# Kernel optimization log

Hardware: AMD Instinct MI355X
Metric: run time of the kernel (lower is better)

## Reference

```python
import jax, jax.numpy as jnp
import numpy as np
from jax import lax

SIZE = 1024
INPUT_DIM = 1024
T = 8192
FORGET_BIAS = 1.0  # BasicLSTMCell default


def setup_inputs() -> dict:
    key = jax.random.key(0)
    k1, k2 = jax.random.split(key)
    x = jax.random.normal(k1, (T, INPUT_DIM), dtype=jnp.float32)
    # BasicLSTMCell kernel: [input_dim + size, 4*size], gate order [i, j, f, o]
    W = jax.random.normal(k2, (INPUT_DIM + SIZE, 4 * SIZE), dtype=jnp.float32) * 0.02
    b = jnp.zeros((4 * SIZE,), dtype=jnp.float32)
    return {"x": x, "W": W, "b": b}


def reference(x, W, b):
    size = b.shape[0] // 4
    c0 = jnp.zeros((size,), dtype=x.dtype)
    h0 = jnp.zeros((size,), dtype=x.dtype)

    def step(carry, xt):
        c, h = carry
        # concat([x_t, h_{t-1}]) @ W + b, split into 4 gates [i, j, f, o]
        z = jnp.concatenate([xt, h]) @ W + b
        i, j, f, o = jnp.split(z, 4)
        new_c = c * jax.nn.sigmoid(f + FORGET_BIAS) + jax.nn.sigmoid(i) * jnp.tanh(j)
        new_h = jnp.tanh(new_c) * jax.nn.sigmoid(o)
        return (new_c, new_h), new_h

    _, hs = lax.scan(step, (c0, h0), x)
    # tf.reshape(rnn, [-1, size]) -> [T, size]
    return hs
```

## Files before the change

kernel.cpp:

```cpp
#include <hip/hip_runtime.h>
#include <hip/hip_fp16.h>
#include <math.h>

#define T_STEPS 8192
#define IN_DIM  1024
#define HD      1024
#define ZD      4096
#define G2      64
#define B2      512

typedef short  short8 __attribute__((ext_vector_type(8)));
typedef float  f32x4  __attribute__((ext_vector_type(4)));
typedef unsigned uint4v __attribute__((ext_vector_type(4)));
typedef _Float16 h2v __attribute__((ext_vector_type(2)));

__device__ __forceinline__ unsigned short f2bf(float f) {
    unsigned u = __float_as_uint(f);
    unsigned r = (u + 0x7fffu + ((u >> 16) & 1u)) >> 16;
    return (unsigned short)r;
}

__device__ __forceinline__ unsigned pk16(float a, float b) {
    return __builtin_bit_cast(unsigned, __builtin_amdgcn_cvt_pkrtz(a, b));
}

__global__ void wt_pack(const float* __restrict__ W, unsigned short* __restrict__ Wt) {
    int idx = blockIdx.x * 256 + threadIdx.x;
    int k = idx >> 12;
    int c = idx & 4095;
    float v = W[(size_t)k * ZD + c];
    int tn = c >> 7, col = c & 127;
    int tk = k >> 5, kk = k & 31;
    Wt[(((size_t)(tn * 32 + tk) * 128 + col) << 5) + kk] = f2bf(v);
}

__global__ void whp_pack(const float* __restrict__ W, unsigned* __restrict__ Whp) {
    int i = blockIdx.x * 256 + threadIdx.x;
    int zcol = i & 4095;
    int seg  = i >> 12;
    const float* src = W + (size_t)(IN_DIM + (seg << 7)) * ZD + zcol;
    unsigned* dst = Whp + ((size_t)zcol * 8 + seg) * 64;
    for (int j = 0; j < 64; ++j) {
        float v0 = src[(size_t)(2 * j) * ZD];
        float v1 = src[(size_t)(2 * j + 1) * ZD];
        unsigned lo = (unsigned)__half_as_ushort(__float2half(v0));
        unsigned hi = (unsigned)__half_as_ushort(__float2half(v1));
        dst[j] = lo | (hi << 16);
    }
}

#define BM 128
#define BN 128
#define BKK 32
#define LDA 40

__global__ __launch_bounds__(256) void zx_gemm(const float* __restrict__ x,
                                               const unsigned short* __restrict__ Wt,
                                               const float* __restrict__ b,
                                               float* __restrict__ zx) {
    __shared__ unsigned short As[128 * LDA];
    __shared__ unsigned short Bs[128 * LDA];
    const int tid  = threadIdx.x;
    const int wave = tid >> 6, lane = tid & 63;
    const int wr = wave & 1, wc = wave >> 1;
    const int m0 = blockIdx.y * BM, n0 = blockIdx.x * BN;
    const int quad = lane >> 4, l16 = lane & 15;

    f32x4 acc[4][4] = {};
    float bias[4];
#pragma unroll
    for (int j = 0; j < 4; ++j) bias[j] = b[n0 + wc * 64 + j * 16 + l16];

    for (int it = 0; it < IN_DIM / BKK; ++it) {
        const int k0 = it * BKK;
        {
            int r  = tid >> 3;
            int k4 = (tid & 7) * 4;
#pragma unroll
            for (int p = 0; p < 4; ++p) {
                int rr = r + p * 32;
                float4 v = *(const float4*)&x[(size_t)(m0 + rr) * IN_DIM + k0 + k4];
                unsigned p0 = (unsigned)f2bf(v.x) | ((unsigned)f2bf(v.y) << 16);
                unsigned p1 = (unsigned)f2bf(v.z) | ((unsigned)f2bf(v.w) << 16);
                *(uint2*)&As[rr * LDA + k4] = make_uint2(p0, p1);
            }
        }
        {
            const uint4* src = (const uint4*)(Wt + ((size_t)(n0 >> 7) * 32 + it) * 4096);
#pragma unroll
            for (int p = 0; p < 2; ++p) {
                int id = tid * 2 + p;
                int col = id >> 2, kp = id & 3;
                uint4 v = src[id];
                *(uint4*)&Bs[col * LDA + kp * 8] = v;
            }
        }
        __syncthreads();
        short8 af[4], bfr[4];
#pragma unroll
        for (int i = 0; i < 4; ++i)
            af[i] = *(const short8*)&As[(wr * 64 + i * 16 + l16) * LDA + quad * 8];
#pragma unroll
        for (int j = 0; j < 4; ++j)
            bfr[j] = *(const short8*)&Bs[(wc * 64 + j * 16 + l16) * LDA + quad * 8];
#pragma unroll
        for (int i = 0; i < 4; ++i)
#pragma unroll
            for (int j = 0; j < 4; ++j)
                acc[i][j] = __builtin_amdgcn_mfma_f32_16x16x32_bf16(af[i], bfr[j], acc[i][j], 0, 0, 0);
        __syncthreads();
    }
#pragma unroll
    for (int i = 0; i < 4; ++i) {
        int row = m0 + wr * 64 + i * 16 + quad * 4;
#pragma unroll
        for (int j = 0; j < 4; ++j) {
            int col = n0 + wc * 64 + j * 16 + l16;
#pragma unroll
            for (int r = 0; r < 4; ++r)
                zx[(size_t)(row + r) * ZD + col] = acc[i][j][r] + bias[j];
        }
    }
}

__device__ __forceinline__ float sigmoid_fast(float x) {
    float e = __expf(-x);
    return __builtin_amdgcn_rcpf(1.f + e);
}
__device__ __forceinline__ float tanh_fast(float x) {
    float e = __expf(2.f * x);
    return 1.f - 2.f * __builtin_amdgcn_rcpf(e + 1.f);
}

__global__ __launch_bounds__(B2, 2) void lstm_seq(const unsigned* __restrict__ whp,
                                                  const float* __restrict__ zx,
                                                  float* __restrict__ out,
                                                  unsigned* hslot) {
    __shared__ unsigned lds_hh[512];
    __shared__ float pbuf[2][B2];
    __shared__ float zx_lds[2][64];
    const int g    = blockIdx.x;
    const int t    = threadIdx.x;
    const int seg  = t >> 6;
    const int lane = t & 63;
    const int gate = lane >> 4;
    const int cidx = lane & 15;
    const int zcol = g * 16 + cidx + (gate << 10);

    unsigned wp[64];
    {
        const unsigned* wsrc = whp + ((size_t)zcol * 8 + seg) * 64;
#pragma unroll
        for (int j = 0; j < 64; ++j) wp[j] = wsrc[j];
    }
#pragma unroll
    for (int j = 0; j < 64; ++j) asm volatile("" : "+v"(wp[j]));

    if (t >= 64 && t < 128) {
        int l = t - 64;
        zx_lds[0][l] = zx[(size_t)0 * ZD + (size_t)(l >> 4) * 1024 + g * 16 + (l & 15)];
    }
    __syncthreads();

    float c_state = 0.f;

    for (int s = 0; s < T_STEPS; ++s) {
        const int par = s & 1;
        float znext = 0.f;
        if (t >= 64 && t < 128 && s + 1 < T_STEPS) {
            int l = t - 64;
            znext = zx[(size_t)(s + 1) * ZD + (size_t)(l >> 4) * 1024 + g * 16 + (l & 15)];
        }
        if (lane < 32) {
            const unsigned want = (unsigned)(s & 255);
            const unsigned* ap = hslot + (par << 10) + (seg << 7) + (lane << 2);
            uint4v pv;
            for (;;) {
                asm volatile("global_load_dwordx4 %0, %1, off sc0 sc1\n\t"
                             "s_waitcnt vmcnt(0)"
                             : "=v"(pv) : "v"(ap) : "memory");
                unsigned bad = ((pv.x ^ want) | (pv.y ^ want) |
                                (pv.z ^ want) | (pv.w ^ want)) & 255u;
                if (bad == 0) break;
            }
            unsigned d0 = pk16(__uint_as_float(pv.x), __uint_as_float(pv.y));
            unsigned d1 = pk16(__uint_as_float(pv.z), __uint_as_float(pv.w));
            *(uint2*)&lds_hh[(seg << 6) + 2 * lane] = make_uint2(d0, d1);
        }
        float a0 = 0.f, a1 = 0.f, a2 = 0.f, a3 = 0.f;
        const uint4* hp = (const uint4*)&lds_hh[seg << 6];
#pragma unroll
        for (int j = 0; j < 16; ++j) {
            uint4 hv = hp[j];
            a0 = __builtin_amdgcn_fdot2(__builtin_bit_cast(h2v, wp[4 * j + 0]),
                                        __builtin_bit_cast(h2v, hv.x), a0, false);
            a1 = __builtin_amdgcn_fdot2(__builtin_bit_cast(h2v, wp[4 * j + 1]),
                                        __builtin_bit_cast(h2v, hv.y), a1, false);
            a2 = __builtin_amdgcn_fdot2(__builtin_bit_cast(h2v, wp[4 * j + 2]),
                                        __builtin_bit_cast(h2v, hv.z), a2, false);
            a3 = __builtin_amdgcn_fdot2(__builtin_bit_cast(h2v, wp[4 * j + 3]),
                                        __builtin_bit_cast(h2v, hv.w), a3, false);
        }
        pbuf[par][t] = (a0 + a1) + (a2 + a3);
        if (t >= 64 && t < 128)
            zx_lds[(s + 1) & 1][t - 64] = znext;
        __syncthreads();
        if (t < 64) {
            float z = zx_lds[s & 1][t];
#pragma unroll
            for (int ss = 0; ss < 8; ++ss) z += pbuf[par][(ss << 6) + t];
            float zi = __shfl(z, cidx);
            float zj = __shfl(z, 16 + cidx);
            float zf = __shfl(z, 32 + cidx);
            float zo = __shfl(z, 48 + cidx);
            if (t < 16) {
                float fg = sigmoid_fast(zf + 1.0f);
                float ig = sigmoid_fast(zi);
                float og = sigmoid_fast(zo);
                c_state = c_state * fg + ig * tanh_fast(zj);
                float h = tanh_fast(c_state) * og;
                unsigned hb  = (__float_as_uint(h) + 0x80u) & 0xFFFFFF00u;
                unsigned pkt = hb | (unsigned)((s + 1) & 255);
                __hip_atomic_store(hslot + (((s + 1) & 1) << 10) + g * 16 + t, pkt,
                                   __ATOMIC_RELAXED, __HIP_MEMORY_SCOPE_AGENT);
                out[(size_t)s * HD + g * 16 + t] = h;
            }
        }
    }
}

extern "C" void kernel_launch(void* const* d_in, const int* in_sizes, int n_in,
                              void* d_out, int out_size, void* d_ws, size_t ws_size,
                              hipStream_t stream) {
    const float* x = (const float*)d_in[0];
    const float* W = (const float*)d_in[1];
    const float* b = (const float*)d_in[2];
    float* out = (float*)d_out;

    char* ws = (char*)d_ws;
    float*          zxp   = (float*)ws;
    const size_t    ZXB   = (size_t)T_STEPS * ZD * sizeof(float);
    unsigned*       hslot = (unsigned*)(ws + ZXB);
    unsigned short* Wt    = (unsigned short*)(ws + ZXB + 16384);
    unsigned*       Whp   = (unsigned*)(ws + ZXB + 16384);

    hipMemsetAsync(hslot, 0, 8192, stream);

    wt_pack<<<dim3((IN_DIM * ZD) / 256), dim3(256), 0, stream>>>(W, Wt);

    zx_gemm<<<dim3(ZD / BN, T_STEPS / BM), dim3(256), 0, stream>>>(x, Wt, b, zxp);

    whp_pack<<<dim3(128), dim3(256), 0, stream>>>(W, Whp);

    void* args[] = { (void*)&Whp, (void*)&zxp, (void*)&out, (void*)&hslot };
    hipLaunchCooperativeKernel((void*)lstm_seq, dim3(G2), dim3(B2), args, 0, stream);
}
```

Before: 12.24 ms.

## Pin recurrent LSTM workgroups to a single XCC and use non-coherent local sync

Launches 512 cooperative workgroups that each read their hardware XCC ID, agree through a global table, and keep only 64 workgroups that share one XCC. Those run a variant whose flag polling and h-slot stores use sc0-only (XCC-local) cache scope instead of system/agent scope. The goal is to cut the cross-die coherence latency of the per-step handoff between workgroups. It adds a startup election barrier, a spin timeout that can silently drop work, and relies on occupancy to fit 512 blocks; if that fails it falls back to the old 64-block launch.

```diff
diff --git a/kernel.cpp b/kernel.cpp
--- a/kernel.cpp
+++ b/kernel.cpp
@@ -7,6 +7,7 @@
 #define HD      1024
 #define ZD      4096
 #define G2      64
+#define NWG     512
 #define B2      512
 
 typedef short  short8 __attribute__((ext_vector_type(8)));
@@ -132,15 +133,12 @@
     return 1.f - 2.f * __builtin_amdgcn_rcpf(e + 1.f);
 }
 
-__global__ __launch_bounds__(B2, 2) void lstm_seq(const unsigned* __restrict__ whp,
-                                                  const float* __restrict__ zx,
-                                                  float* __restrict__ out,
-                                                  unsigned* hslot) {
-    __shared__ unsigned lds_hh[512];
-    __shared__ float pbuf[2][B2];
-    __shared__ float zx_lds[2][64];
-    const int g    = blockIdx.x;
-    const int t    = threadIdx.x;
+template<bool LOCAL>
+__device__ __forceinline__ void lstm_loop(int g, const unsigned* __restrict__ whp,
+                                          const float* __restrict__ zx,
+                                          float* __restrict__ out, unsigned* hslot,
+                                          unsigned* lds_hh, float (*pbuf)[B2],
+                                          float (*zx_lds)[64], int t) {
     const int seg  = t >> 6;
     const int lane = t & 63;
     const int gate = lane >> 4;
@@ -153,8 +151,6 @@
 #pragma unroll
         for (int j = 0; j < 64; ++j) wp[j] = wsrc[j];
     }
-#pragma unroll
-    for (int j = 0; j < 64; ++j) asm volatile("" : "+v"(wp[j]));
 
     if (t >= 64 && t < 128) {
         int l = t - 64;
@@ -163,6 +159,7 @@
     __syncthreads();
 
     float c_state = 0.f;
+    int alive = 1;
 
     for (int s = 0; s < T_STEPS; ++s) {
         const int par = s & 1;
@@ -171,17 +168,24 @@
             int l = t - 64;
             znext = zx[(size_t)(s + 1) * ZD + (size_t)(l >> 4) * 1024 + g * 16 + (l & 15)];
         }
-        if (lane < 32) {
+        if (lane < 32 && alive) {
             const unsigned want = (unsigned)(s & 255);
             const unsigned* ap = hslot + (par << 10) + (seg << 7) + (lane << 2);
             uint4v pv;
+            int it = 0;
             for (;;) {
-                asm volatile("global_load_dwordx4 %0, %1, off sc0 sc1\n\t"
-                             "s_waitcnt vmcnt(0)"
-                             : "=v"(pv) : "v"(ap) : "memory");
+                if constexpr (LOCAL)
+                    asm volatile("global_load_dwordx4 %0, %1, off sc0\n\t"
+                                 "s_waitcnt vmcnt(0)"
+                                 : "=v"(pv) : "v"(ap) : "memory");
+                else
+                    asm volatile("global_load_dwordx4 %0, %1, off sc0 sc1\n\t"
+                                 "s_waitcnt vmcnt(0)"
+                                 : "=v"(pv) : "v"(ap) : "memory");
                 unsigned bad = ((pv.x ^ want) | (pv.y ^ want) |
                                 (pv.z ^ want) | (pv.w ^ want)) & 255u;
                 if (bad == 0) break;
+                if (++it > (1 << 22)) { alive = 0; break; }
             }
             unsigned d0 = pk16(__uint_as_float(pv.x), __uint_as_float(pv.y));
             unsigned d1 = pk16(__uint_as_float(pv.z), __uint_as_float(pv.w));
@@ -221,12 +225,83 @@
                 float h = tanh_fast(c_state) * og;
                 unsigned hb  = (__float_as_uint(h) + 0x80u) & 0xFFFFFF00u;
                 unsigned pkt = hb | (unsigned)((s + 1) & 255);
-                __hip_atomic_store(hslot + (((s + 1) & 1) << 10) + g * 16 + t, pkt,
-                                   __ATOMIC_RELAXED, __HIP_MEMORY_SCOPE_AGENT);
+                unsigned* pp = hslot + (((s + 1) & 1) << 10) + g * 16 + t;
+                if constexpr (LOCAL)
+                    asm volatile("global_store_dword %0, %1, off sc0"
+                                 :: "v"(pp), "v"(pkt) : "memory");
+                else
+                    __hip_atomic_store(pp, pkt, __ATOMIC_RELAXED,
+                                       __HIP_MEMORY_SCOPE_AGENT);
                 out[(size_t)s * HD + g * 16 + t] = h;
             }
         }
     }
+}
+
+__global__ __launch_bounds__(B2, 4) void lstm_seq(const unsigned* __restrict__ whp,
+                                                  const float* __restrict__ zx,
+                                                  float* __restrict__ out,
+                                                  unsigned* hslot,
+                                                  int* xtab, int* cnt) {
+    __shared__ unsigned lds_hh[512];
+    __shared__ float pbuf[2][B2];
+    __shared__ float zx_lds[2][64];
+    __shared__ int xcc_lds[NWG];
+    __shared__ int sel[2];
+    const int t = threadIdx.x, bid = blockIdx.x;
+    int mode, g;
+
+    if ((int)gridDim.x >= NWG) {
+        if (t == 0) {
+            unsigned xcc;
+            asm volatile("s_getreg_b32 %0, hwreg(HW_REG_XCC_ID)" : "=s"(xcc));
+            __hip_atomic_store(&xtab[bid], (int)(xcc & 7) | 256, __ATOMIC_RELAXED,
+                               __HIP_MEMORY_SCOPE_AGENT);
+            __hip_atomic_fetch_add(cnt, 1, __ATOMIC_RELEASE, __HIP_MEMORY_SCOPE_AGENT);
+            int it = 0;
+            while (__hip_atomic_load(cnt, __ATOMIC_ACQUIRE,
+                                     __HIP_MEMORY_SCOPE_AGENT) < (int)gridDim.x)
+                if (++it > (1 << 22)) break;
+        }
+        __syncthreads();
+        if (t < NWG)
+            xcc_lds[t] = __hip_atomic_load(&xtab[t], __ATOMIC_RELAXED,
+                                           __HIP_MEMORY_SCOPE_AGENT);
+        __syncthreads();
+        if (t == 0) {
+            int counts[8] = {};
+            bool valid = true;
+            for (int j = 0; j < NWG; ++j) {
+                int v = xcc_lds[j];
+                if (!(v & 256)) valid = false;
+                counts[v & 7]++;
+            }
+            int target = -1;
+            if (valid)
+                for (int xc = 0; xc < 8; ++xc)
+                    if (counts[xc] >= G2) { target = xc; break; }
+            if (target >= 0) {
+                int mine = xcc_lds[bid] & 7;
+                int rank = 0;
+                for (int j = 0; j < bid; ++j) if ((xcc_lds[j] & 7) == mine) rank++;
+                sel[0] = (mine == target && rank < G2) ? 1 : 0;
+                sel[1] = rank;
+            } else {
+                sel[0] = (bid < G2) ? 2 : 0;
+                sel[1] = bid;
+            }
+        }
+        __syncthreads();
+        if (sel[0] == 0) return;
+        mode = sel[0];
+        g    = sel[1];
+    } else {
+        mode = 2;
+        g    = bid;
+    }
+
+    if (mode == 1) lstm_loop<true >(g, whp, zx, out, hslot, lds_hh, pbuf, zx_lds, t);
+    else           lstm_loop<false>(g, whp, zx, out, hslot, lds_hh, pbuf, zx_lds, t);
 }
 
 extern "C" void kernel_launch(void* const* d_in, const int* in_sizes, int n_in,
@@ -241,10 +316,12 @@
     float*          zxp   = (float*)ws;
     const size_t    ZXB   = (size_t)T_STEPS * ZD * sizeof(float);
     unsigned*       hslot = (unsigned*)(ws + ZXB);
+    int*            xtab  = (int*)(ws + ZXB + 8192);
+    int*            cnt   = (int*)(ws + ZXB + 8192 + 2048);
     unsigned short* Wt    = (unsigned short*)(ws + ZXB + 16384);
     unsigned*       Whp   = (unsigned*)(ws + ZXB + 16384);
 
-    hipMemsetAsync(hslot, 0, 8192, stream);
+    hipMemsetAsync(hslot, 0, 16384, stream);
 
     wt_pack<<<dim3((IN_DIM * ZD) / 256), dim3(256), 0, stream>>>(W, Wt);
 
@@ -252,6 +329,16 @@
 
     whp_pack<<<dim3(128), dim3(256), 0, stream>>>(W, Whp);
 
-    void* args[] = { (void*)&Whp, (void*)&zxp, (void*)&out, (void*)&hslot };
-    hipLaunchCooperativeKernel((void*)lstm_seq, dim3(G2), dim3(B2), args, 0, stream);
-}
+    void* args[] = { (void*)&Whp, (void*)&zxp, (void*)&out, (void*)&hslot,
+                     (void*)&xtab, (void*)&cnt };
+    int nb = 0;
+    hipError_t qe = hipOccupancyMaxActiveBlocksPerMultiprocessor(
+                        &nb, reinterpret_cast<const void*>(lstm_seq), B2, 0);
+    hipError_t le = hipErrorUnknown;
+    if (qe == hipSuccess && nb >= 2)
+        le = hipLaunchCooperativeKernel((void*)lstm_seq, dim3(NWG), dim3(B2),
+                                        args, 0, stream);
+    if (le != hipSuccess)
+        hipLaunchCooperativeKernel((void*)lstm_seq, dim3(G2), dim3(B2),
+                                   args, 0, stream);
+}
```

New measurement: 12.42 ms. About the same (+1.5%).
